# Kernel optimization log

Hardware: AMD Instinct MI355X
Metric: run time of the kernel (lower is better)

The kernel has to match this reference:

```python
import jax, jax.numpy as jnp
import numpy as np

WEMD, TAGSET, TEMD, RANK = 400, 50, 20, 396
SEQ, BATCH = 512, 32


def setup_inputs() -> dict:
    key = jax.random.key(0)
    ks = jax.random.split(key, 7)
    std = 0.1545
    return {
        "word_emd": jax.random.normal(ks[0], (SEQ, BATCH, WEMD), dtype=jnp.float32),
        "tag_emd": jax.random.normal(ks[1], (TAGSET, TEMD), dtype=jnp.float32) * std,
        "T": jax.random.normal(ks[2], (WEMD, RANK), dtype=jnp.float32) * std,
        "U": jax.random.normal(ks[3], (WEMD, RANK), dtype=jnp.float32) * std,
        "V": jax.random.normal(ks[4], (TEMD, RANK), dtype=jnp.float32) * std,
        "W": jax.random.normal(ks[5], (TEMD, RANK), dtype=jnp.float32) * std,
        "first_wemb": jax.random.normal(ks[6], (1, WEMD), dtype=jnp.float32) * std,
    }


def reference(word_emd, tag_emd, T, U, V, W, first_wemb):
    # neighbor == 'prev': shift word embeddings right by one along seq,
    # prepending the learned first_wemb broadcast over batch.
    seq, batch, wemd = word_emd.shape
    first = jnp.broadcast_to(first_wemb.reshape(1, 1, wemd), (1, batch, wemd))
    neighbor_word_emd = jnp.concatenate([first, word_emd[:-1]], axis=0)  # [n,a,w]

    g0 = jnp.matmul(word_emd, U)          # [n,a,k]
    g1 = jnp.matmul(neighbor_word_emd, T) # [n,a,k]
    g2 = jnp.matmul(tag_emd, V)           # [b,k]
    g3 = jnp.matmul(tag_emd, W)           # [c,k]

    # Fused quadrilinear contraction: avoids materializing [n,a,b,k]
    # (same math as einsum('nak,bk->nabk') then 'nabk,ck->nabc').
    score = jnp.einsum('nak,bk,ck->nabc', g0 * g1, g2, g3)
    return score
```

## Files before the change

### kernel.cpp

```cpp
#include <hip/hip_runtime.h>

typedef unsigned short u16;
typedef __bf16 bf16x8 __attribute__((ext_vector_type(8)));
typedef float f32x4 __attribute__((ext_vector_type(4)));

#define WEMD 400
#define RANK 396
#define NA   16384
#define KP   416
#define K2   448
#define BSTR 896
#define NBC  2500
#define NBCP 2560

#define OFF_WBF  0u
#define OFF_UBT  13658112u
#define OFF_TBT  14084096u
#define OFF_G    14689280u
#define OFF_H    16983040u

__device__ __forceinline__ u16 f2bf(float f) {
  union { float f; unsigned u; } v; v.f = f;
  unsigned u = v.u;
  return (u16)((u + 0x7FFFu + ((u >> 16) & 1u)) >> 16);
}

typedef __attribute__((address_space(3))) unsigned char lds_byte;
typedef __attribute__((address_space(1))) const unsigned char glob_byte;

__device__ __forceinline__ void gload16(const void* g, void* l) {
  __builtin_amdgcn_global_load_lds((glob_byte*)g, (lds_byte*)l, 16, 0, 0);
}

__global__ __launch_bounds__(256) void prep_all(
    const float* __restrict__ word, const float* __restrict__ first,
    const float* __restrict__ U, const float* __restrict__ T,
    const float* __restrict__ tag, const float* __restrict__ V,
    const float* __restrict__ W,
    u16* __restrict__ Wbf, u16* __restrict__ Ubt, u16* __restrict__ Tbt,
    u16* __restrict__ G) {
  const int R0 = 16416 * 104;
  const int R1 = 416 << 9;
  const int R2 = NBCP * K2;
  const int total = R0 + R1 + R2;
  for (int i = blockIdx.x * 256 + threadIdx.x; i < total; i += gridDim.x * 256) {
    if (i < R0) {
      int r = i / 104, c4 = i - r * 104;
      ushort4 o = {0, 0, 0, 0};
      if (c4 < 100) {
        const float* src = (r < 32) ? (first + c4 * 4)
                                    : (word + (size_t)(r - 32) * WEMD + c4 * 4);
        float4 v = *(const float4*)src;
        o.x = f2bf(v.x); o.y = f2bf(v.y); o.z = f2bf(v.z); o.w = f2bf(v.w);
      }
      *(ushort4*)(Wbf + (size_t)r * KP + c4 * 4) = o;
    } else if (i < R0 + R1) {
      int j = i - R0;
      int n = j & 511, k = j >> 9;
      u16 uo = 0, to = 0;
      if (n < RANK && k < WEMD) {
        uo = f2bf(U[(size_t)k * RANK + n]);
        to = f2bf(T[(size_t)k * RANK + n]);
      }
      Ubt[(size_t)n * KP + k] = uo;
      Tbt[(size_t)n * KP + k] = to;
    } else {
      int j = i - R0 - R1;
      int bc = j / K2, k = j - bc * K2;
      u16 g = 0;
      if (bc < NBC && k < RANK) {
        int b = bc / 50, c = bc - b * 50;
        float a2 = 0.f, a3 = 0.f;
        #pragma unroll
        for (int e = 0; e < 20; ++e) {
          a2 += tag[b * 20 + e] * V[e * RANK + k];
          a3 += tag[c * 20 + e] * W[e * RANK + k];
        }
        g = f2bf(a2 * a3);
      }
      G[(size_t)bc * K2 + k] = g;
    }
  }
}

__global__ __launch_bounds__(256) void gemm_h(const u16* __restrict__ Wbf,
                                              const u16* __restrict__ Ubt,
                                              const u16* __restrict__ Tbt,
                                              u16* __restrict__ H) {
  __shared__ u16 As0[128 * 32], As1[128 * 32], Bu[128 * 32], Bt[128 * 32];
  const int tid = threadIdx.x;
  const int l = tid & 63, w = tid >> 6;
  const int wm = w >> 1, wn = w & 1;
  const int tm = (blockIdx.x >> 2) * 128, tn = (blockIdx.x & 3) * 128;

  f32x4 acc0[4][4] = {}, acc1[4][4] = {};

  const int srow = tid >> 2;
  const int scolb = (tid & 3) * 16;
  const char* gA0 = (const char*)Wbf + (size_t)(tm + 32 + srow) * 832 + scolb;
  const char* gA1 = (const char*)Wbf + (size_t)(tm + srow) * 832 + scolb;
  const char* gU  = (const char*)Ubt + (size_t)(tn + srow) * 832 + scolb;
  const char* gT  = (const char*)Tbt + (size_t)(tn + srow) * 832 + scolb;
  char* lA0 = (char*)As0 + tid * 16;
  char* lA1 = (char*)As1 + tid * 16;
  char* lU  = (char*)Bu  + tid * 16;
  char* lT  = (char*)Bt  + tid * 16;

  const int fo_a = (wm * 64 + (l & 15)) * 32 + (l >> 4) * 8;
  const int fo_b = (wn * 64 + (l & 15)) * 32 + (l >> 4) * 8;

  for (int kt = 0; kt < 13; ++kt) {
    const int kb = kt * 64;
    gload16(gA0 + kb, lA0); gload16(gA0 + kb + (size_t)64 * 832, lA0 + 4096);
    gload16(gA1 + kb, lA1); gload16(gA1 + kb + (size_t)64 * 832, lA1 + 4096);
    gload16(gU  + kb, lU ); gload16(gU  + kb + (size_t)64 * 832, lU  + 4096);
    gload16(gT  + kb, lT ); gload16(gT  + kb + (size_t)64 * 832, lT  + 4096);
    __syncthreads();
    bf16x8 a0[4], a1[4], bu[4], bt[4];
    #pragma unroll
    for (int i = 0; i < 4; ++i) {
      a0[i] = *(const bf16x8*)(As0 + fo_a + i * 16 * 32);
      a1[i] = *(const bf16x8*)(As1 + fo_a + i * 16 * 32);
      bu[i] = *(const bf16x8*)(Bu  + fo_b + i * 16 * 32);
      bt[i] = *(const bf16x8*)(Bt  + fo_b + i * 16 * 32);
    }
    #pragma unroll
    for (int i = 0; i < 4; ++i)
      #pragma unroll
      for (int j = 0; j < 4; ++j) {
        acc0[i][j] = __builtin_amdgcn_mfma_f32_16x16x32_bf16(a0[i], bu[j], acc0[i][j], 0, 0, 0);
        acc1[i][j] = __builtin_amdgcn_mfma_f32_16x16x32_bf16(a1[i], bt[j], acc1[i][j], 0, 0, 0);
      }
    __syncthreads();
  }

  const int r4 = (l >> 4) * 4, cc = l & 15;
  #pragma unroll
  for (int i = 0; i < 4; ++i)
    #pragma unroll
    for (int j = 0; j < 4; ++j) {
      const int col = tn + wn * 64 + j * 16 + cc;
      if (col < K2) {
        #pragma unroll
        for (int r = 0; r < 4; ++r) {
          const int rowg = tm + wm * 64 + i * 16 + r4 + r;
          H[(size_t)rowg * K2 + col] = f2bf(acc0[i][j][r] * acc1[i][j][r]);
        }
      }
    }
}

__global__ __launch_bounds__(256, 3) void gemm_big2(const u16* __restrict__ H,
                                                    const u16* __restrict__ G,
                                                    float* __restrict__ out) {
  __shared__ u16 lds[2 * 8192];
  char* ldsb = (char*)lds;
  const int tid = threadIdx.x;
  const int lane = tid & 63, wid = tid >> 6;
  const int wm = wid >> 1, wn = wid & 1;

  int bs = (int)blockIdx.x;
  bs = (bs & 7) * 320 + (bs >> 3);
  const int tm = (bs / 20) * 128, tn = (bs % 20) * 128;

  const char* gH = (const char*)H + (size_t)tm * BSTR;
  const char* gG = (const char*)G + (size_t)tn * BSTR;

  int sP[4], sR[4], sC[4];
  #pragma unroll
  for (int q = 0; q < 4; ++q) {
    int P = tid * 16 + q * 4096;
    int L = P ^ (((P >> 7) & 7) << 4);
    sP[q] = P; sR[q] = L >> 7; sC[q] = L & 127;
  }
  const int arow = (lane & 15) * 128;
  const int sw = (lane & 7) << 4;

  f32x4 acc[4][4] = {};

  for (int kt = 0; kt < 7; ++kt) {
    const int kb = kt * 128;
    #pragma unroll
    for (int q = 0; q < 4; ++q) {
      gload16(gH + (size_t)sR[q] * BSTR + kb + sC[q], ldsb + sP[q]);
      gload16(gG + (size_t)sR[q] * BSTR + kb + sC[q], ldsb + 16384 + sP[q]);
    }
    __syncthreads();
    #pragma unroll
    for (int ks = 0; ks < 2; ++ks) {
      const int csw = (ks * 64 + (lane >> 4) * 16) ^ sw;
      bf16x8 a[4], b[4];
      #pragma unroll
      for (int rf = 0; rf < 4; ++rf)
        a[rf] = *(const bf16x8*)(ldsb + wm * 8192 + rf * 2048 + arow + csw);
      #pragma unroll
      for (int cf = 0; cf < 4; ++cf)
        b[cf] = *(const bf16x8*)(ldsb + 16384 + wn * 8192 + cf * 2048 + arow + csw);
      #pragma unroll
      for (int rf = 0; rf < 4; ++rf)
        #pragma unroll
        for (int cf = 0; cf < 4; ++cf)
          acc[rf][cf] = __builtin_amdgcn_mfma_f32_16x16x32_bf16(a[rf], b[cf], acc[rf][cf], 0, 0, 0);
    }
    __syncthreads();
  }

  const int r4 = (lane >> 4) * 4, cc = lane & 15;
  const int rbase = tm + wm * 64 + r4;
  const int cbase = tn + wn * 64 + cc;
  #pragma unroll
  for (int rf = 0; rf < 4; ++rf)
    #pragma unroll
    for (int cf = 0; cf < 4; ++cf) {
      const int col = cbase + cf * 16;
      if (col < NBC) {
        #pragma unroll
        for (int rr = 0; rr < 4; ++rr)
          out[(size_t)(rbase + rf * 16 + rr) * NBC + col] = acc[rf][cf][rr];
      }
    }
}

extern "C" void kernel_launch(void* const* d_in, const int* in_sizes, int n_in,
                              void* d_out, int out_size, void* d_ws, size_t ws_size,
                              hipStream_t stream) {
  const float* word  = (const float*)d_in[0];
  const float* tag   = (const float*)d_in[1];
  const float* Tm    = (const float*)d_in[2];
  const float* Um    = (const float*)d_in[3];
  const float* Vm    = (const float*)d_in[4];
  const float* Wm    = (const float*)d_in[5];
  const float* first = (const float*)d_in[6];
  float* out = (float*)d_out;
  char* ws = (char*)d_ws;

  u16*   Wbf = (u16*)(ws + OFF_WBF);
  u16*   Ubt = (u16*)(ws + OFF_UBT);
  u16*   Tbt = (u16*)(ws + OFF_TBT);
  u16*   G   = (u16*)(ws + OFF_G);
  u16*   H   = (u16*)(ws + OFF_H);

  hipLaunchKernelGGL(prep_all, dim3(2048), dim3(256), 0, stream,
                     word, first, Um, Tm, tag, Vm, Wm, Wbf, Ubt, Tbt, G);
  hipLaunchKernelGGL(gemm_h,   dim3(128 * 4), dim3(256), 0, stream, Wbf, Ubt, Tbt, H);
  hipLaunchKernelGGL(gemm_big2, dim3(2560), dim3(256), 0, stream, H, G, out);
}
```

Measured before the change: 115.6 us.

## Double-buffer LDS tiles in main GEMM to overlap loads with MFMA

The second GEMM kernel now keeps two LDS buffers. It prefetches the next K-tile with global_load_lds while MFMAs run on the current tile, and uses explicit vmcnt waits plus raw barriers in place of __syncthreads. This hides global load latency behind compute. In exchange, LDS use per block doubles to 64KB, and the occupancy hint drops from 3 to 2 blocks per CU, so fewer waves are available to hide latency.

```diff
diff --git a/kernel.cpp b/kernel.cpp
--- a/kernel.cpp
+++ b/kernel.cpp
@@ -31,6 +31,10 @@
 __device__ __forceinline__ void gload16(const void* g, void* l) {
   __builtin_amdgcn_global_load_lds((glob_byte*)g, (lds_byte*)l, 16, 0, 0);
 }
+
+#define FENCE() asm volatile("" ::: "memory")
+#define BARRIER() do { FENCE(); __builtin_amdgcn_s_barrier(); FENCE(); } while (0)
+#define VMCNT0() asm volatile("s_waitcnt vmcnt(0)" ::: "memory")
 
 __global__ __launch_bounds__(256) void prep_all(
     const float* __restrict__ word, const float* __restrict__ first,
@@ -150,10 +154,10 @@
     }
 }
 
-__global__ __launch_bounds__(256, 3) void gemm_big2(const u16* __restrict__ H,
+__global__ __launch_bounds__(256, 2) void gemm_big2(const u16* __restrict__ H,
                                                     const u16* __restrict__ G,
                                                     float* __restrict__ out) {
-  __shared__ u16 lds[2 * 8192];
+  __shared__ u16 lds[4 * 8192];
   char* ldsb = (char*)lds;
   const int tid = threadIdx.x;
   const int lane = tid & 63, wid = tid >> 6;
@@ -178,31 +182,49 @@
 
   f32x4 acc[4][4] = {};
 
+  #pragma unroll
+  for (int q = 0; q < 4; ++q) {
+    gload16(gH + (size_t)sR[q] * BSTR + sC[q], ldsb + sP[q]);
+    gload16(gG + (size_t)sR[q] * BSTR + sC[q], ldsb + 16384 + sP[q]);
+  }
+  VMCNT0();
+  BARRIER();
+
   for (int kt = 0; kt < 7; ++kt) {
-    const int kb = kt * 128;
-    #pragma unroll
-    for (int q = 0; q < 4; ++q) {
-      gload16(gH + (size_t)sR[q] * BSTR + kb + sC[q], ldsb + sP[q]);
-      gload16(gG + (size_t)sR[q] * BSTR + kb + sC[q], ldsb + 16384 + sP[q]);
-    }
-    __syncthreads();
+    const int cur = kt & 1;
+    char* cbuf = ldsb + cur * 32768;
+
+    if (kt < 6) {
+      char* nbuf = ldsb + (cur ^ 1) * 32768;
+      const int kb = (kt + 1) * 128;
+      #pragma unroll
+      for (int q = 0; q < 4; ++q) {
+        gload16(gH + (size_t)sR[q] * BSTR + kb + sC[q], nbuf + sP[q]);
+        gload16(gG + (size_t)sR[q] * BSTR + kb + sC[q], nbuf + 16384 + sP[q]);
+      }
+    }
+
     #pragma unroll
     for (int ks = 0; ks < 2; ++ks) {
       const int csw = (ks * 64 + (lane >> 4) * 16) ^ sw;
       bf16x8 a[4], b[4];
       #pragma unroll
       for (int rf = 0; rf < 4; ++rf)
-        a[rf] = *(const bf16x8*)(ldsb + wm * 8192 + rf * 2048 + arow + csw);
+        a[rf] = *(const bf16x8*)(cbuf + wm * 8192 + rf * 2048 + arow + csw);
       #pragma unroll
       for (int cf = 0; cf < 4; ++cf)
-        b[cf] = *(const bf16x8*)(ldsb + 16384 + wn * 8192 + cf * 2048 + arow + csw);
+        b[cf] = *(const bf16x8*)(cbuf + 16384 + wn * 8192 + cf * 2048 + arow + csw);
       #pragma unroll
       for (int rf = 0; rf < 4; ++rf)
         #pragma unroll
         for (int cf = 0; cf < 4; ++cf)
           acc[rf][cf] = __builtin_amdgcn_mfma_f32_16x16x32_bf16(a[rf], b[cf], acc[rf][cf], 0, 0, 0);
     }
-    __syncthreads();
+
+    if (kt < 6) {
+      VMCNT0();
+      BARRIER();
+    }
   }
 
   const int r4 = (lane >> 4) * 4, cc = lane & 15;
```

Result: slower. 120.5 us (+4.3%).

## Replace big GEMM with persistent kernel keeping H rows resident in LDS

Applied to the files above, without the earlier changes.

The second GEMM becomes a persistent kernel with 256 blocks of 512 threads. Each block loads its full 128-row H slab (all K) into LDS once and then walks 10 column tiles of G, double-buffering G tiles with explicit vmcnt waits and raw barriers so loads overlap MFMA work. This removes the repeated re-reads of H across column tiles and the launch/tail cost of 2560 small blocks. In exchange it uses about 144KB of LDS per block, which limits occupancy, and it relies on hand-tuned vmcnt counts that must match the number of issued loads.

```diff
diff --git a/kernel.cpp b/kernel.cpp
--- a/kernel.cpp
+++ b/kernel.cpp
@@ -31,6 +31,12 @@
 __device__ __forceinline__ void gload16(const void* g, void* l) {
   __builtin_amdgcn_global_load_lds((glob_byte*)g, (lds_byte*)l, 16, 0, 0);
 }
+
+#define FENCE() asm volatile("" ::: "memory")
+#define BARRIER() do { FENCE(); __builtin_amdgcn_s_barrier(); FENCE(); } while (0)
+#define VMCNT0()  asm volatile("s_waitcnt vmcnt(0)"  ::: "memory")
+#define VMCNT2()  asm volatile("s_waitcnt vmcnt(2)"  ::: "memory")
+#define VMCNT34() asm volatile("s_waitcnt vmcnt(34)" ::: "memory")
 
 __global__ __launch_bounds__(256) void prep_all(
     const float* __restrict__ word, const float* __restrict__ first,
@@ -150,75 +156,106 @@
     }
 }
 
-__global__ __launch_bounds__(256, 3) void gemm_big2(const u16* __restrict__ H,
+#define STAGEG(ntg, ktc, bsel)                                                     \
+  do {                                                                             \
+    _Pragma("unroll")                                                              \
+    for (int q = 0; q < 2; ++q) {                                                  \
+      int P = tid * 16 + q * 8192;                                                 \
+      int row = P >> 7;                                                            \
+      int col = (P & 127) ^ ((row & 7) << 4);                                      \
+      gload16(gG + (size_t)((ntg) * 128 + row) * BSTR + (ktc) * 128 + col,         \
+              ldsb + 114688 + (bsel) * 16384 + P);                                 \
+    }                                                                              \
+  } while (0)
+
+__global__ __launch_bounds__(512, 2) void gemm_pers(const u16* __restrict__ H,
                                                     const u16* __restrict__ G,
                                                     float* __restrict__ out) {
-  __shared__ u16 lds[2 * 8192];
+  __shared__ u16 lds[73728];
   char* ldsb = (char*)lds;
   const int tid = threadIdx.x;
   const int lane = tid & 63, wid = tid >> 6;
-  const int wm = wid >> 1, wn = wid & 1;
+  const int wm = wid >> 2, wn = wid & 3;
 
   int bs = (int)blockIdx.x;
-  bs = (bs & 7) * 320 + (bs >> 3);
-  const int tm = (bs / 20) * 128, tn = (bs % 20) * 128;
-
-  const char* gH = (const char*)H + (size_t)tm * BSTR;
-  const char* gG = (const char*)G + (size_t)tn * BSTR;
-
-  int sP[4], sR[4], sC[4];
+  bs = (bs & 7) * 32 + (bs >> 3);
+  const int tm = (bs >> 1) * 128;
+  const int nt0 = (bs & 1) * 10;
+
+  const char* gH = (const char*)H;
+  const char* gG = (const char*)G;
+
   #pragma unroll
-  for (int q = 0; q < 4; ++q) {
-    int P = tid * 16 + q * 4096;
-    int L = P ^ (((P >> 7) & 7) << 4);
-    sP[q] = P; sR[q] = L >> 7; sC[q] = L & 127;
-  }
-  const int arow = (lane & 15) * 128;
+  for (int q = 0; q < 14; ++q) {
+    int P = tid * 16 + q * 8192;
+    int row = P / 896;
+    int colp = P - row * 896;
+    int col = colp ^ ((row & 7) << 4);
+    gload16(gH + (size_t)(tm + row) * BSTR + col, ldsb + P);
+  }
+  STAGEG(nt0, 0, 0);
+  VMCNT0();
+  BARRIER();
+
+  const int al = lane & 15;
+  const int ah = (lane >> 4) * 16;
   const int sw = (lane & 7) << 4;
-
-  f32x4 acc[4][4] = {};
-
-  for (int kt = 0; kt < 7; ++kt) {
-    const int kb = kt * 128;
-    #pragma unroll
-    for (int q = 0; q < 4; ++q) {
-      gload16(gH + (size_t)sR[q] * BSTR + kb + sC[q], ldsb + sP[q]);
-      gload16(gG + (size_t)sR[q] * BSTR + kb + sC[q], ldsb + 16384 + sP[q]);
-    }
-    __syncthreads();
-    #pragma unroll
-    for (int ks = 0; ks < 2; ++ks) {
-      const int csw = (ks * 64 + (lane >> 4) * 16) ^ sw;
-      bf16x8 a[4], b[4];
+  const int r4 = (lane >> 4) * 4;
+
+  f32x4 acc[4][2] = {};
+  int buf = 0;
+
+  for (int nt = 0; nt < 10; ++nt) {
+    for (int kt = 0; kt < 7; ++kt) {
+      const bool last = (nt == 9) && (kt == 6);
+      if (!last) {
+        int nkt = kt + 1, nnt = nt;
+        if (nkt == 7) { nkt = 0; nnt = nt + 1; }
+        STAGEG(nt0 + nnt, nkt, buf ^ 1);
+      }
+      if (last)                { VMCNT0(); }
+      else if (kt == 0 && nt)  { VMCNT34(); }
+      else                     { VMCNT2();  }
+      BARRIER();
+
       #pragma unroll
-      for (int rf = 0; rf < 4; ++rf)
-        a[rf] = *(const bf16x8*)(ldsb + wm * 8192 + rf * 2048 + arow + csw);
-      #pragma unroll
-      for (int cf = 0; cf < 4; ++cf)
-        b[cf] = *(const bf16x8*)(ldsb + 16384 + wn * 8192 + cf * 2048 + arow + csw);
-      #pragma unroll
-      for (int rf = 0; rf < 4; ++rf)
-        #pragma unroll
-        for (int cf = 0; cf < 4; ++cf)
-          acc[rf][cf] = __builtin_amdgcn_mfma_f32_16x16x32_bf16(a[rf], b[cf], acc[rf][cf], 0, 0, 0);
-    }
-    __syncthreads();
-  }
-
-  const int r4 = (lane >> 4) * 4, cc = lane & 15;
-  const int rbase = tm + wm * 64 + r4;
-  const int cbase = tn + wn * 64 + cc;
-  #pragma unroll
-  for (int rf = 0; rf < 4; ++rf)
-    #pragma unroll
-    for (int cf = 0; cf < 4; ++cf) {
-      const int col = cbase + cf * 16;
-      if (col < NBC) {
-        #pragma unroll
-        for (int rr = 0; rr < 4; ++rr)
-          out[(size_t)(rbase + rf * 16 + rr) * NBC + col] = acc[rf][cf][rr];
-      }
-    }
+      for (int ks = 0; ks < 2; ++ks) {
+        const int ca = (kt * 128 + ks * 64 + ah) ^ sw;
+        const int cb = (ks * 64 + ah) ^ sw;
+        bf16x8 a[4], bv[2];
+        #pragma unroll
+        for (int rf = 0; rf < 4; ++rf)
+          a[rf] = *(const bf16x8*)(ldsb + (size_t)(wm * 64 + rf * 16 + al) * BSTR + ca);
+        #pragma unroll
+        for (int cf = 0; cf < 2; ++cf)
+          bv[cf] = *(const bf16x8*)(ldsb + 114688 + buf * 16384 +
+                                    (wn * 32 + cf * 16 + al) * 128 + cb);
+        #pragma unroll
+        for (int rf = 0; rf < 4; ++rf)
+          #pragma unroll
+          for (int cf = 0; cf < 2; ++cf)
+            acc[rf][cf] = __builtin_amdgcn_mfma_f32_16x16x32_bf16(a[rf], bv[cf], acc[rf][cf], 0, 0, 0);
+      }
+      BARRIER();
+      buf ^= 1;
+
+      if (kt == 6) {
+        const int colb = (nt0 + nt) * 128 + wn * 32 + al;
+        #pragma unroll
+        for (int rf = 0; rf < 4; ++rf)
+          #pragma unroll
+          for (int cf = 0; cf < 2; ++cf) {
+            const int col = colb + cf * 16;
+            if (col < NBC) {
+              #pragma unroll
+              for (int rr = 0; rr < 4; ++rr)
+                out[(size_t)(tm + wm * 64 + rf * 16 + r4 + rr) * NBC + col] = acc[rf][cf][rr];
+            }
+            acc[rf][cf] = f32x4{0.f, 0.f, 0.f, 0.f};
+          }
+      }
+    }
+  }
 }
 
 extern "C" void kernel_launch(void* const* d_in, const int* in_sizes, int n_in,
@@ -243,5 +280,5 @@
   hipLaunchKernelGGL(prep_all, dim3(2048), dim3(256), 0, stream,
                      word, first, Um, Tm, tag, Vm, Wm, Wbf, Ubt, Tbt, G);
   hipLaunchKernelGGL(gemm_h,   dim3(128 * 4), dim3(256), 0, stream, Wbf, Ubt, Tbt, H);
-  hipLaunchKernelGGL(gemm_big2, dim3(2560), dim3(256), 0, stream, H, G, out);
-}
+  hipLaunchKernelGGL(gemm_pers, dim3(256), dim3(512), 0, stream, H, G, out);
+}
```

New measurement: 117.9 us. +2.1%, slower.

## Fuse word-embedding bf16 conversion into first GEMM and co-schedule G computation

Applied to the files above, without the earlier changes.

Removes the separate bf16 staging copy of the word embeddings. The first GEMM now loads fp32 word rows, and their shifted neighbours, straight into swizzled LDS and converts them to bf16 while building fragments. The G (tag product) computation moves into extra blocks of the same launch, and the U/T transpose becomes its own small kernel. This avoids writing and re-reading a ~13MB bf16 copy, at the cost of twice the LDS traffic for fp32 A tiles and clamped out-of-range loads.

```diff
diff --git a/kernel.cpp b/kernel.cpp
--- a/kernel.cpp
+++ b/kernel.cpp
@@ -13,12 +13,13 @@
 #define NBC  2500
 #define NBCP 2560
 
-#define OFF_WBF  0u
 #define OFF_UBT  13658112u
 #define OFF_TBT  14084096u
 #define OFF_G    14689280u
 #define OFF_H    16983040u
 
+#define WBYTES_MAX 26214384ull
+
 __device__ __forceinline__ u16 f2bf(float f) {
   union { float f; unsigned u; } v; v.f = f;
   unsigned u = v.u;
@@ -32,40 +33,24 @@
   __builtin_amdgcn_global_load_lds((glob_byte*)g, (lds_byte*)l, 16, 0, 0);
 }
 
-__global__ __launch_bounds__(256) void prep_all(
+__global__ void prep_ut(const float* __restrict__ U, const float* __restrict__ T,
+                        u16* __restrict__ Ubt, u16* __restrict__ Tbt) {
+  int idx = blockIdx.x * 256 + threadIdx.x;
+  if (idx >= 512 * KP) return;
+  int n = idx / KP, k = idx - n * KP;
+  u16 uo = 0, to = 0;
+  if (n < RANK && k < WEMD) { uo = f2bf(U[(size_t)k * RANK + n]); to = f2bf(T[(size_t)k * RANK + n]); }
+  Ubt[idx] = uo; Tbt[idx] = to;
+}
+
+__global__ __launch_bounds__(256) void gemm_h2(
     const float* __restrict__ word, const float* __restrict__ first,
-    const float* __restrict__ U, const float* __restrict__ T,
+    const u16* __restrict__ Ubt, const u16* __restrict__ Tbt,
+    u16* __restrict__ H,
     const float* __restrict__ tag, const float* __restrict__ V,
-    const float* __restrict__ W,
-    u16* __restrict__ Wbf, u16* __restrict__ Ubt, u16* __restrict__ Tbt,
-    u16* __restrict__ G) {
-  const int R0 = 16416 * 104;
-  const int R1 = 416 << 9;
-  const int R2 = NBCP * K2;
-  const int total = R0 + R1 + R2;
-  for (int i = blockIdx.x * 256 + threadIdx.x; i < total; i += gridDim.x * 256) {
-    if (i < R0) {
-      int r = i / 104, c4 = i - r * 104;
-      ushort4 o = {0, 0, 0, 0};
-      if (c4 < 100) {
-        const float* src = (r < 32) ? (first + c4 * 4)
-                                    : (word + (size_t)(r - 32) * WEMD + c4 * 4);
-        float4 v = *(const float4*)src;
-        o.x = f2bf(v.x); o.y = f2bf(v.y); o.z = f2bf(v.z); o.w = f2bf(v.w);
-      }
-      *(ushort4*)(Wbf + (size_t)r * KP + c4 * 4) = o;
-    } else if (i < R0 + R1) {
-      int j = i - R0;
-      int n = j & 511, k = j >> 9;
-      u16 uo = 0, to = 0;
-      if (n < RANK && k < WEMD) {
-        uo = f2bf(U[(size_t)k * RANK + n]);
-        to = f2bf(T[(size_t)k * RANK + n]);
-      }
-      Ubt[(size_t)n * KP + k] = uo;
-      Tbt[(size_t)n * KP + k] = to;
-    } else {
-      int j = i - R0 - R1;
+    const float* __restrict__ Wm, u16* __restrict__ G) {
+  if (blockIdx.x >= 512) {
+    for (int j = (blockIdx.x - 512) * 256 + threadIdx.x; j < NBCP * K2; j += 64 * 256) {
       int bc = j / K2, k = j - bc * K2;
       u16 g = 0;
       if (bc < NBC && k < RANK) {
@@ -74,55 +59,79 @@
         #pragma unroll
         for (int e = 0; e < 20; ++e) {
           a2 += tag[b * 20 + e] * V[e * RANK + k];
-          a3 += tag[c * 20 + e] * W[e * RANK + k];
+          a3 += tag[c * 20 + e] * Wm[e * RANK + k];
         }
         g = f2bf(a2 * a3);
       }
       G[(size_t)bc * K2 + k] = g;
     }
-  }
-}
-
-__global__ __launch_bounds__(256) void gemm_h(const u16* __restrict__ Wbf,
-                                              const u16* __restrict__ Ubt,
-                                              const u16* __restrict__ Tbt,
-                                              u16* __restrict__ H) {
-  __shared__ u16 As0[128 * 32], As1[128 * 32], Bu[128 * 32], Bt[128 * 32];
+    return;
+  }
+
+  __shared__ __align__(16) char ldsb[49152];
+  char* ldsAw = ldsb;
+  char* ldsAn = ldsb + 16384;
+  const u16* Bu = (const u16*)(ldsb + 32768);
+  const u16* Bt = (const u16*)(ldsb + 40960);
+
   const int tid = threadIdx.x;
   const int l = tid & 63, w = tid >> 6;
   const int wm = w >> 1, wn = w & 1;
   const int tm = (blockIdx.x >> 2) * 128, tn = (blockIdx.x & 3) * 128;
 
   f32x4 acc0[4][4] = {}, acc1[4][4] = {};
-
-  const int srow = tid >> 2;
-  const int scolb = (tid & 3) * 16;
-  const char* gA0 = (const char*)Wbf + (size_t)(tm + 32 + srow) * 832 + scolb;
-  const char* gA1 = (const char*)Wbf + (size_t)(tm + srow) * 832 + scolb;
-  const char* gU  = (const char*)Ubt + (size_t)(tn + srow) * 832 + scolb;
-  const char* gT  = (const char*)Tbt + (size_t)(tn + srow) * 832 + scolb;
-  char* lA0 = (char*)As0 + tid * 16;
-  char* lA1 = (char*)As1 + tid * 16;
-  char* lU  = (char*)Bu  + tid * 16;
-  char* lT  = (char*)Bt  + tid * 16;
-
-  const int fo_a = (wm * 64 + (l & 15)) * 32 + (l >> 4) * 8;
   const int fo_b = (wn * 64 + (l & 15)) * 32 + (l >> 4) * 8;
 
   for (int kt = 0; kt < 13; ++kt) {
-    const int kb = kt * 64;
-    gload16(gA0 + kb, lA0); gload16(gA0 + kb + (size_t)64 * 832, lA0 + 4096);
-    gload16(gA1 + kb, lA1); gload16(gA1 + kb + (size_t)64 * 832, lA1 + 4096);
-    gload16(gU  + kb, lU ); gload16(gU  + kb + (size_t)64 * 832, lU  + 4096);
-    gload16(gT  + kb, lT ); gload16(gT  + kb + (size_t)64 * 832, lT  + 4096);
-    __syncthreads();
+    const int kb4 = kt * 128;
+    const int kb  = kt * 64;
+    #pragma unroll
+    for (int q = 0; q < 4; ++q) {
+      int P = tid * 16 + q * 4096;
+      int row = P >> 7, colp = P & 127;
+      int col = colp ^ ((row & 7) << 4);
+      size_t offw = (size_t)(tm + row) * 1600 + kb4 + col;
+      if (offw > WBYTES_MAX) offw = WBYTES_MAX;
+      gload16((const char*)word + offw, ldsAw + P);
+      const char* srcn;
+      if (tm + row >= 32) {
+        size_t offn = (size_t)(tm + row - 32) * 1600 + kb4 + col;
+        if (offn > WBYTES_MAX) offn = WBYTES_MAX;
+        srcn = (const char*)word + offn;
+      } else {
+        int offf = kb4 + col; if (offf > 1584) offf = 1584;
+        srcn = (const char*)first + offf;
+      }
+      gload16(srcn, ldsAn + P);
+    }
+    #pragma unroll
+    for (int q = 0; q < 2; ++q) {
+      int P = tid * 16 + q * 4096;
+      int row = P >> 6, colb = P & 63;
+      gload16((const char*)Ubt + (size_t)(tn + row) * 832 + kb + colb, (char*)Bu + P);
+      gload16((const char*)Tbt + (size_t)(tn + row) * 832 + kb + colb, (char*)Bt + P);
+    }
+    __syncthreads();
+
     bf16x8 a0[4], a1[4], bu[4], bt[4];
     #pragma unroll
     for (int i = 0; i < 4; ++i) {
-      a0[i] = *(const bf16x8*)(As0 + fo_a + i * 16 * 32);
-      a1[i] = *(const bf16x8*)(As1 + fo_a + i * 16 * 32);
-      bu[i] = *(const bf16x8*)(Bu  + fo_b + i * 16 * 32);
-      bt[i] = *(const bf16x8*)(Bt  + fo_b + i * 16 * 32);
+      const int ar = wm * 64 + i * 16 + (l & 15);
+      const int swz = (ar & 7) << 4;
+      const int c0 = (l >> 4) * 32;
+      f32x4 w0 = *(const f32x4*)(ldsAw + ar * 128 + (c0 ^ swz));
+      f32x4 w1 = *(const f32x4*)(ldsAw + ar * 128 + ((c0 + 16) ^ swz));
+      f32x4 n0 = *(const f32x4*)(ldsAn + ar * 128 + (c0 ^ swz));
+      f32x4 n1 = *(const f32x4*)(ldsAn + ar * 128 + ((c0 + 16) ^ swz));
+      bf16x8 aw, an;
+      #pragma unroll
+      for (int jj = 0; jj < 4; ++jj) {
+        aw[jj] = (__bf16)w0[jj]; aw[4 + jj] = (__bf16)w1[jj];
+        an[jj] = (__bf16)n0[jj]; an[4 + jj] = (__bf16)n1[jj];
+      }
+      a0[i] = aw; a1[i] = an;
+      bu[i] = *(const bf16x8*)(Bu + fo_b + i * 16 * 32);
+      bt[i] = *(const bf16x8*)(Bt + fo_b + i * 16 * 32);
     }
     #pragma unroll
     for (int i = 0; i < 4; ++i)
@@ -234,14 +243,13 @@
   float* out = (float*)d_out;
   char* ws = (char*)d_ws;
 
-  u16*   Wbf = (u16*)(ws + OFF_WBF);
   u16*   Ubt = (u16*)(ws + OFF_UBT);
   u16*   Tbt = (u16*)(ws + OFF_TBT);
   u16*   G   = (u16*)(ws + OFF_G);
   u16*   H   = (u16*)(ws + OFF_H);
 
-  hipLaunchKernelGGL(prep_all, dim3(2048), dim3(256), 0, stream,
-                     word, first, Um, Tm, tag, Vm, Wm, Wbf, Ubt, Tbt, G);
-  hipLaunchKernelGGL(gemm_h,   dim3(128 * 4), dim3(256), 0, stream, Wbf, Ubt, Tbt, H);
+  hipLaunchKernelGGL(prep_ut,  dim3((512 * KP + 255) / 256), dim3(256), 0, stream, Um, Tm, Ubt, Tbt);
+  hipLaunchKernelGGL(gemm_h2,  dim3(576), dim3(256), 0, stream,
+                     word, first, Ubt, Tbt, H, tag, Vm, Wm, G);
   hipLaunchKernelGGL(gemm_big2, dim3(2560), dim3(256), 0, stream, H, G, out);
 }
```

Result: slower. 163.3 us (+41.4%).
